# Kernel tuning notes

Hardware: AMD Instinct MI355X
Metric: run time of the kernel (lower is better)

Reference implementation:

```python
import jax, jax.numpy as jnp
import numpy as np

N_HEAD = 8


def setup_inputs() -> dict:
    key = jax.random.key(0)
    ks = jax.random.split(key, 8)
    v, b, c, h, w = 8, 4, 512, 16, 16
    s = 1.0 / np.sqrt(c).astype(np.float32)
    return {
        "q": jax.random.normal(ks[0], (v, b, c, h, w), jnp.float32),
        "kv": jax.random.normal(ks[1], (v, b, c, h, w), jnp.float32),
        "Wq": jax.random.normal(ks[2], (c, c), jnp.float32) * s,
        "bq": jnp.zeros((c,), jnp.float32),
        "Wkv": jax.random.normal(ks[3], (c, 2 * c), jnp.float32) * s,
        "bkv": jnp.zeros((2 * c,), jnp.float32),
        "Wp": jax.random.normal(ks[4], (c, c), jnp.float32) * s,
        "bp": jnp.zeros((c,), jnp.float32),
    }


def reference(q, kv, Wq, bq, Wkv, bkv, Wp, bp):
    vi, bi, ci, hi, wi = q.shape
    hw = hi * wi
    T = vi * hw
    hd = ci // N_HEAD

    # rearrange 'v b c h w -> b (v h w) c'
    xq = q.transpose(1, 0, 3, 4, 2).reshape(bi, T, ci)
    xkv = kv.transpose(1, 0, 3, 4, 2).reshape(bi, T, ci)

    qp = xq @ Wq + bq                      # [b, T, c]
    k, v_ = jnp.split(xkv @ Wkv + bkv, 2, axis=-1)

    def heads(x):
        return x.reshape(bi, T, N_HEAD, hd).transpose(0, 2, 1, 3)  # [b,h,T,d]

    qh, kh, vh = heads(qp), heads(k), heads(v_)

    att = jnp.einsum('bhqd,bhkd->bhqk', qh, kh) * (1.0 / np.sqrt(hd).astype(np.float32))

    # block-causal mask: query block (size h*w) may attend to key blocks <= its own
    blocks = jnp.arange(T) // hw
    mask = blocks[:, None] >= blocks[None, :]
    att = jnp.where(mask, att, -jnp.inf)
    att = jax.nn.softmax(att, axis=-1)

    y = jnp.einsum('bhqk,bhkd->bhqd', att, vh)
    y = y.transpose(0, 2, 1, 3).reshape(bi, T, ci)
    y = y @ Wp + bp

    # rearrange 'b (v h w) c -> v b c h w'
    return y.reshape(bi, vi, hi, wi, ci).transpose(1, 0, 4, 2, 3)
```

## Files before the change

kernel.cpp:

```cpp
#include <hip/hip_runtime.h>
#include <hip/hip_bf16.h>
#include <cmath>

typedef unsigned short u16;
typedef __attribute__((ext_vector_type(8))) short s8v;
typedef __attribute__((ext_vector_type(4))) float f4v;
typedef __attribute__((ext_vector_type(2))) float f2v;
typedef __attribute__((ext_vector_type(4))) unsigned int u32x4;
typedef __attribute__((ext_vector_type(4))) unsigned short u16x4;

#define MFMA(a,b,c) __builtin_amdgcn_mfma_f32_16x16x32_bf16((a),(b),(c),0,0,0)

__device__ __forceinline__ float bf2f(u16 u) {
    union { float f; unsigned i; } x; x.i = ((unsigned)u) << 16; return x.f;
}
__device__ __forceinline__ u16 f2bf(float f) {
    union { float f; unsigned i; } x; x.f = f;
    unsigned r = x.i + 0x7FFFu + ((x.i >> 16) & 1u);
    return (u16)(r >> 16);
}
__device__ __forceinline__ unsigned cvtpk(float lo, float hi) {
    unsigned r;
    asm("v_cvt_pk_bf16_f32 %0, %1, %2" : "=v"(r) : "v"(lo), "v"(hi));
    return r;
}
__device__ __forceinline__ void gload_lds16(const void* g, void* l) {
    __builtin_amdgcn_global_load_lds(
        (const __attribute__((address_space(1))) unsigned int*)g,
        (__attribute__((address_space(3))) unsigned int*)l, 16, 0, 0);
}
__device__ __forceinline__ int swb(int row, int colb) {
    return row * 128 + (colb ^ ((((row >> 4) ^ row) & 7) << 4));
}

__constant__ int CPER[8]  = {1,1,2,2,3,3,4,4};
__constant__ int POFF[17] = {0,1,2,3,4,6,8,10,12,15,18,21,24,28,32,36,40};

__global__ __launch_bounds__(256, 3)
void qkv_proj(const float* __restrict__ q, const float* __restrict__ kv,
              const float* __restrict__ Wq, const float* __restrict__ bq,
              const float* __restrict__ Wkv, const float* __restrict__ bkv,
              u16* __restrict__ QH, u16* __restrict__ KH, u16* __restrict__ VT)
{
    __shared__ __align__(16) u16 Tl[2][128 * 64];

    const int bid = blockIdx.x;
    const int x = bid & 7, i = bid >> 3;
    const int mt = x + 8 * (i / 12);
    const int nt = i % 12;
    const int m0 = mt << 7, n0 = nt << 7;

    const int tid  = threadIdx.x;
    const int lane = tid & 63;
    const int w    = tid >> 6;
    const int wr = (w >> 1) * 64, wc = (w & 1) * 64;
    const int cl = lane & 15, rl = lane >> 4;

    const int bb  = m0 >> 11;
    const int t0  = m0 & 2047;
    const int vv  = t0 >> 8;
    const int hw0 = t0 & 255;

    const float* Abase = ((nt < 4) ? q : kv) + (size_t)(vv * 4 + bb) * 131072 + hw0;

    const float* W; const float* bias; int NW, wn0, dn0; u16* dst;
    if (nt < 4)      { W = Wq;  bias = bq;  NW = 512;  wn0 = n0;       dn0 = n0;        dst = QH; }
    else if (nt < 8) { W = Wkv; bias = bkv; NW = 1024; wn0 = n0 - 512; dn0 = n0 - 512;  dst = KH; }
    else             { W = Wkv; bias = bkv; NW = 1024; wn0 = n0 - 512; dn0 = n0 - 1024; dst = VT; }

    const float oscale = (nt < 4) ? 0.18033688011f : 1.0f;

    f4v acc[4][4] = {};
    f2v la0[8], lb0[8], la1[8], lb1[8];

    const int mh = tid & 63;
    const int kb = tid >> 6;

#define QKV_LOAD(dA, dB, k0_) do {                                           \
        const float* gA = Abase + (size_t)((k0_) + kb * 8) * 256 + mh * 2;   \
        const float* gB = W + (size_t)((k0_) + kb * 8) * NW + wn0 + mh * 2;  \
        _Pragma("unroll")                                                    \
        for (int j = 0; j < 8; ++j) {                                        \
            dA[j] = *reinterpret_cast<const f2v*>(gA + j * 256);             \
            dB[j] = *reinterpret_cast<const f2v*>(gB + (size_t)j * NW);      \
        }                                                                    \
    } while (0)

#define QKV_WRITE(bufi, sA, sB) do {                                         \
        _Pragma("unroll")                                                    \
        for (int e = 0; e < 2; ++e) {                                        \
            u32x4 pa, pb;                                                    \
            _Pragma("unroll")                                                \
            for (int jj = 0; jj < 4; ++jj) {                                 \
                pa[jj] = cvtpk(sA[jj * 2][e], sA[jj * 2 + 1][e]);            \
                pb[jj] = cvtpk(sB[jj * 2][e], sB[jj * 2 + 1][e]);            \
            }                                                                \
            *(u32x4*)((char*)&Tl[bufi][0] + swb(mh * 2 + e, kb * 16)) = pa;  \
            *(u32x4*)((char*)&Tl[bufi][0] + swb(mh * 2 + e, 64 + kb * 16)) = pb; \
        }                                                                    \
    } while (0)

#define QKV_MFMA(bufi) do {                                                  \
        s8v af[4], bf[4];                                                    \
        _Pragma("unroll")                                                    \
        for (int mi = 0; mi < 4; ++mi)                                       \
            af[mi] = *(const s8v*)((const char*)&Tl[bufi][0]                 \
                                   + swb(wr + mi * 16 + cl, rl * 16));       \
        _Pragma("unroll")                                                    \
        for (int ni = 0; ni < 4; ++ni)                                       \
            bf[ni] = *(const s8v*)((const char*)&Tl[bufi][0]                 \
                                   + swb(wc + ni * 16 + cl, 64 + rl * 16));  \
        _Pragma("unroll")                                                    \
        for (int mi = 0; mi < 4; ++mi)                                       \
            _Pragma("unroll")                                                \
            for (int ni = 0; ni < 4; ++ni)                                   \
                acc[mi][ni] = MFMA(af[mi], bf[ni], acc[mi][ni]);             \
    } while (0)

    QKV_LOAD(la0, lb0, 0);
    QKV_WRITE(0, la0, lb0);
    QKV_LOAD(la1, lb1, 32);
    __syncthreads();

    #pragma unroll
    for (int it = 0; it < 8; ++it) {
        const int t = it * 2;
        QKV_WRITE(1, la1, lb1);
        if (t + 2 < 16) QKV_LOAD(la0, lb0, (t + 2) * 32);
        QKV_MFMA(0);
        __syncthreads();
        if (t + 2 < 16) QKV_WRITE(0, la0, lb0);
        if (t + 3 < 16) QKV_LOAD(la1, lb1, (t + 3) * 32);
        QKV_MFMA(1);
        __syncthreads();
    }
#undef QKV_LOAD
#undef QKV_WRITE
#undef QKV_MFMA

    if (nt < 8) {
        #pragma unroll
        for (int ni = 0; ni < 4; ++ni) {
            const int nl   = wc + ni * 16 + cl;
            const float bv = bias[wn0 + nl];
            const int cout = dn0 + nl;
            const int hh = cout >> 6, dd = cout & 63;
            const size_t obase = ((size_t)(bb * 8 + hh) * 2048) * 64 + dd;
            #pragma unroll
            for (int mi = 0; mi < 4; ++mi)
                #pragma unroll
                for (int r = 0; r < 4; ++r) {
                    const int m = m0 + wr + mi * 16 + rl * 4 + r;
                    const int t = m & 2047;
                    dst[obase + (size_t)t * 64] = f2bf((acc[mi][ni][r] + bv) * oscale);
                }
        }
    } else {
        #pragma unroll
        for (int ni = 0; ni < 4; ++ni) {
            const int nl   = wc + ni * 16 + cl;
            const float bv = bias[wn0 + nl];
            const int cout = dn0 + nl;
            const int hh = cout >> 6, dd = cout & 63;
            const size_t obase = ((size_t)(bb * 8 + hh) * 64 + dd) * 2048;
            #pragma unroll
            for (int mi = 0; mi < 4; ++mi) {
                const int m = m0 + wr + mi * 16 + rl * 4;
                const int t = m & 2047;
                u16x4 pk;
                #pragma unroll
                for (int r = 0; r < 4; ++r) pk[r] = f2bf(acc[mi][ni][r] + bv);
                *reinterpret_cast<u16x4*>(dst + obase + t) = pk;
            }
        }
    }
}

__global__ __launch_bounds__(256, 3)
void attn_part(const u16* __restrict__ QH, const u16* __restrict__ KH,
               const u16* __restrict__ VT,
               u16* __restrict__ Opart, float* __restrict__ ML)
{
    __shared__ __align__(16) u16 Kl[2][4096];
    __shared__ __align__(16) u16 Vl[2][4096];
    __shared__ u16 Pl[4][32][36];

    const int wg = blockIdx.x;
    const int bh = wg & 31;
    const int s  = 39 - (wg >> 5);
    int p = 0;
    #pragma unroll
    for (int i = 0; i < 15; ++i) p += (s >= POFF[i + 1]) ? 1 : 0;
    const int c  = s - POFF[p];
    const int qb = p >> 1;
    const int kstart = c * 512;
    const int nk = min(512, (qb + 1) * 256 - kstart);
    const int nt64 = nk >> 6;

    const int tid = threadIdx.x, lane = tid & 63, w = tid >> 6;
    const int cl = lane & 15, rl = lane >> 4;

    const u16* Qb = QH + (size_t)bh * 131072;
    const u16* Kb = KH + (size_t)bh * 131072;
    const u16* Vb = VT + (size_t)bh * 131072;

    const int qrow0 = p * 128 + w * 32;

    s8v qf[2][2];
    #pragma unroll
    for (int mi = 0; mi < 2; ++mi)
        #pragma unroll
        for (int kf = 0; kf < 2; ++kf)
            qf[mi][kf] = *reinterpret_cast<const s8v*>(
                Qb + (size_t)(qrow0 + mi * 16 + cl) * 64 + kf * 32 + rl * 8);

    unsigned kofs[2], vofs[2];
    #pragma unroll
    for (int i = 0; i < 2; ++i) {
        const int f = w * 128 + i * 64 + lane;
        const int row = f >> 3;
        kofs[i] = row * 128 + (((f & 7) * 16) ^ ((row & 7) << 4));
        vofs[i] = row * 4096 + (((f & 7) * 16) ^ ((row & 7) << 4));
    }

#define ISSUE(bufi, kb0_) do {                                               \
        const char* kG = (const char*)Kb + (size_t)(kb0_) * 128;             \
        const char* vG = (const char*)Vb + (size_t)(kb0_) * 2;               \
        char* kL = (char*)&Kl[bufi][0] + w * 2048;                           \
        char* vL = (char*)&Vl[bufi][0] + w * 2048;                           \
        _Pragma("unroll")                                                    \
        for (int i_ = 0; i_ < 2; ++i_) {                                     \
            gload_lds16(kG + kofs[i_], kL + i_ * 1024);                      \
            gload_lds16(vG + vofs[i_], vL + i_ * 1024);                      \
        }                                                                    \
    } while (0)

    f4v o[2][4] = {};
    float lp[8] = {0.f, 0.f, 0.f, 0.f, 0.f, 0.f, 0.f, 0.f};

    ISSUE(0, kstart);

    for (int kt = 0; kt < nt64; ++kt) {
        asm volatile("s_waitcnt vmcnt(0)" ::: "memory");
        __builtin_amdgcn_sched_barrier(0);
        __syncthreads();
        if (kt + 1 < nt64) ISSUE((kt + 1) & 1, kstart + (kt + 1) * 64);

        const char* Kbase = (const char*)&Kl[kt & 1][0];
        const char* Vbase = (const char*)&Vl[kt & 1][0];

        f4v sc[2][4] = {};
        #pragma unroll
        for (int ni = 0; ni < 4; ++ni)
            #pragma unroll
            for (int kf = 0; kf < 2; ++kf) {
                const int row = ni * 16 + cl;
                s8v kfr = *reinterpret_cast<const s8v*>(
                    Kbase + row * 128 + ((kf * 64 + rl * 16) ^ ((row & 7) << 4)));
                sc[0][ni] = MFMA(qf[0][kf], kfr, sc[0][ni]);
                sc[1][ni] = MFMA(qf[1][kf], kfr, sc[1][ni]);
            }

        #pragma unroll
        for (int mi = 0; mi < 2; ++mi)
            #pragma unroll
            for (int ni = 0; ni < 4; ++ni)
                #pragma unroll
                for (int r = 0; r < 4; ++r)
                    sc[mi][ni][r] = exp2f(sc[mi][ni][r]);
        #pragma unroll
        for (int mi = 0; mi < 2; ++mi)
            #pragma unroll
            for (int r = 0; r < 4; ++r)
                lp[mi * 4 + r] += sc[mi][0][r] + sc[mi][1][r]
                                + sc[mi][2][r] + sc[mi][3][r];

        #pragma unroll
        for (int kw = 0; kw < 2; ++kw) {
            #pragma unroll
            for (int mi = 0; mi < 2; ++mi)
                #pragma unroll
                for (int jj = 0; jj < 2; ++jj) {
                    const int ni = kw * 2 + jj;
                    const unsigned w0 = cvtpk(sc[mi][ni][0], sc[mi][ni][1]);
                    const unsigned w1 = cvtpk(sc[mi][ni][2], sc[mi][ni][3]);
                    const int col = jj * 16 + cl;
                    Pl[w][mi * 16 + rl * 4 + 0][col] = (u16)w0;
                    Pl[w][mi * 16 + rl * 4 + 1][col] = (u16)(w0 >> 16);
                    Pl[w][mi * 16 + rl * 4 + 2][col] = (u16)w1;
                    Pl[w][mi * 16 + rl * 4 + 3][col] = (u16)(w1 >> 16);
                }
            s8v pf0 = *reinterpret_cast<const s8v*>(&Pl[w][cl][rl * 8]);
            s8v pf1 = *reinterpret_cast<const s8v*>(&Pl[w][16 + cl][rl * 8]);
            #pragma unroll
            for (int di = 0; di < 4; ++di) {
                const int row = di * 16 + cl;
                s8v vf = *reinterpret_cast<const s8v*>(
                    Vbase + row * 128 + ((kw * 64 + rl * 16) ^ ((row & 7) << 4)));
                o[0][di] = MFMA(pf0, vf, o[0][di]);
                o[1][di] = MFMA(pf1, vf, o[1][di]);
            }
        }
    }
#undef ISSUE

    const int slot = bh * 40 + POFF[p] + c;
    #pragma unroll
    for (int mi = 0; mi < 2; ++mi)
        #pragma unroll
        for (int r = 0; r < 4; ++r) {
            const int idx = mi * 4 + r;
            float ls = lp[idx];
            ls += __shfl_xor(ls, 1);
            ls += __shfl_xor(ls, 2);
            ls += __shfl_xor(ls, 4);
            ls += __shfl_xor(ls, 8);
            const float inv = 1.f / ls;
            const int rloc = w * 32 + mi * 16 + rl * 4 + r;
            if (cl == 0) ML[(size_t)slot * 128 + rloc] = ls;
            #pragma unroll
            for (int di = 0; di < 4; ++di)
                Opart[(size_t)slot * 8192 + rloc * 64 + di * 16 + cl] =
                    f2bf(o[mi][di][r] * inv);
        }
}

__global__ __launch_bounds__(256)
void attn_combine(const u16* __restrict__ Opart, const float* __restrict__ ML,
                  u16* __restrict__ YH)
{
    const int wg = blockIdx.x;
    const int bh = wg & 31;
    const int p  = wg >> 5;
    const int b = bh >> 3, h = bh & 7;
    const int nc = CPER[p >> 1];
    const int sb = bh * 40 + POFF[p];

    const int t = threadIdx.x;
    const int rloc = t >> 1;
    const int dh = (t & 1) * 32;

    float lc[4], L = 0.f;
    for (int c = 0; c < nc; ++c) {
        lc[c] = ML[(size_t)(sb + c) * 128 + rloc];
        L += lc[c];
    }
    const float invL = 1.f / L;
    float wgt[4];
    for (int c = 0; c < nc; ++c) wgt[c] = lc[c] * invL;

    f4v a[8] = {};
    for (int c = 0; c < nc; ++c) {
        const float wv = wgt[c];
        #pragma unroll
        for (int u = 0; u < 4; ++u) {
            s8v vv = *reinterpret_cast<const s8v*>(
                &Opart[(size_t)(sb + c) * 8192 + rloc * 64 + dh + u * 8]);
            #pragma unroll
            for (int e = 0; e < 4; ++e) a[u * 2][e]     += wv * bf2f((u16)vv[e]);
            #pragma unroll
            for (int e = 0; e < 4; ++e) a[u * 2 + 1][e] += wv * bf2f((u16)vv[e + 4]);
        }
    }

    const size_t ybase = ((size_t)b * 2048 + p * 128 + rloc) * 512 + h * 64 + dh;
    #pragma unroll
    for (int u = 0; u < 4; ++u) {
        s8v ov;
        #pragma unroll
        for (int e = 0; e < 4; ++e) ov[e]     = (short)f2bf(a[u * 2][e]);
        #pragma unroll
        for (int e = 0; e < 4; ++e) ov[e + 4] = (short)f2bf(a[u * 2 + 1][e]);
        *reinterpret_cast<s8v*>(YH + ybase + u * 8) = ov;
    }
}

__global__ __launch_bounds__(256)
void out_proj(const u16* __restrict__ YH, const float* __restrict__ Wp,
              const float* __restrict__ bp, float* __restrict__ out)
{
    __shared__ __align__(16) u16 Al[2][128 * 64];
    __shared__ u16 Bl[2][128][40];

    const int bid = blockIdx.x;
    const int x = bid & 7, i = bid >> 3;
    const int mt = x + 8 * (i >> 2);
    const int ct = i & 3;
    const int c0 = ct << 7, m0 = mt << 7;

    const int tid = threadIdx.x, lane = tid & 63, w = tid >> 6;
    const int wr = (w >> 1) * 64, wc = (w & 1) * 64;
    const int cl = lane & 15, rl = lane >> 4;

    f4v acc[4][4] = {};
    f2v wa0[8], wa1[8];
    s8v sy0[2], sy1[2];

    const int mh = tid & 63;
    const int kb = tid >> 6;
    const int br = tid >> 2;
    const int bq4 = (tid & 3) * 8;

#define OP_LOAD(dA, dY, k0_) do {                                            \
        const float* gA = Wp + (size_t)((k0_) + kb * 8) * 512 + c0 + mh * 2; \
        _Pragma("unroll")                                                    \
        for (int j = 0; j < 8; ++j)                                          \
            dA[j] = *reinterpret_cast<const f2v*>(gA + j * 512);             \
        _Pragma("unroll")                                                    \
        for (int it = 0; it < 2; ++it)                                       \
            dY[it] = *reinterpret_cast<const s8v*>(                          \
                YH + (size_t)(m0 + br + it * 64) * 512 + (k0_) + bq4);       \
    } while (0)

#define OP_WRITE(bufi, sA, sY) do {                                          \
        _Pragma("unroll")                                                    \
        for (int e = 0; e < 2; ++e) {                                        \
            u32x4 pa;                                                        \
            _Pragma("unroll")                                                \
            for (int jj = 0; jj < 4; ++jj)                                   \
                pa[jj] = cvtpk(sA[jj * 2][e], sA[jj * 2 + 1][e]);            \
            *(u32x4*)((char*)&Al[bufi][0] + swb(mh * 2 + e, kb * 16)) = pa;  \
        }                                                                    \
        _Pragma("unroll")                                                    \
        for (int it = 0; it < 2; ++it)                                       \
            *reinterpret_cast<s8v*>(&Bl[bufi][br + it * 64][bq4]) = sY[it];  \
    } while (0)

#define OP_MFMA(bufi) do {                                                   \
        s8v af[4], bfr[4];                                                   \
        _Pragma("unroll")                                                    \
        for (int mi = 0; mi < 4; ++mi)                                       \
            af[mi] = *(const s8v*)((const char*)&Al[bufi][0]                 \
                                   + swb(wr + mi * 16 + cl, rl * 16));       \
        _Pragma("unroll")                                                    \
        for (int ni = 0; ni < 4; ++ni)                                       \
            bfr[ni] = *reinterpret_cast<const s8v*>(                         \
                &Bl[bufi][wc + ni * 16 + cl][rl * 8]);                       \
        _Pragma("unroll")                                                    \
        for (int mi = 0; mi < 4; ++mi)                                       \
            _Pragma("unroll")                                                \
            for (int ni = 0; ni < 4; ++ni)                                   \
                acc[mi][ni] = MFMA(af[mi], bfr[ni], acc[mi][ni]);            \
    } while (0)

    OP_LOAD(wa0, sy0, 0);
    OP_WRITE(0, wa0, sy0);
    OP_LOAD(wa1, sy1, 32);
    __syncthreads();

    #pragma unroll
    for (int it = 0; it < 8; ++it) {
        const int t = it * 2;
        OP_WRITE(1, wa1, sy1);
        if (t + 2 < 16) OP_LOAD(wa0, sy0, (t + 2) * 32);
        OP_MFMA(0);
        __syncthreads();
        if (t + 2 < 16) OP_WRITE(0, wa0, sy0);
        if (t + 3 < 16) OP_LOAD(wa1, sy1, (t + 3) * 32);
        OP_MFMA(1);
        __syncthreads();
    }
#undef OP_LOAD
#undef OP_WRITE
#undef OP_MFMA

    #pragma unroll
    for (int mi = 0; mi < 4; ++mi)
        #pragma unroll
        for (int r = 0; r < 4; ++r) {
            const int c = c0 + wr + mi * 16 + rl * 4 + r;
            const float bv = bp[c];
            #pragma unroll
            for (int ni = 0; ni < 4; ++ni) {
                const int tok = m0 + wc + ni * 16 + cl;
                const int bb = tok >> 11, t = tok & 2047;
                const int vv = t >> 8, hw = t & 255;
                out[(size_t)(vv * 4 + bb) * 131072 + (size_t)c * 256 + hw] =
                    acc[mi][ni][r] + bv;
            }
        }
}

extern "C" void kernel_launch(void* const* d_in, const int* in_sizes, int n_in,
                              void* d_out, int out_size, void* d_ws, size_t ws_size,
                              hipStream_t stream)
{
    const float* q   = (const float*)d_in[0];
    const float* kv  = (const float*)d_in[1];
    const float* Wq  = (const float*)d_in[2];
    const float* bq  = (const float*)d_in[3];
    const float* Wkv = (const float*)d_in[4];
    const float* bkv = (const float*)d_in[5];
    const float* Wp  = (const float*)d_in[6];
    const float* bp  = (const float*)d_in[7];
    float* out = (float*)d_out;

    u16* ws = (u16*)d_ws;
    u16* QH = ws;
    u16* KH = QH + 4194304;
    u16* VT = KH + 4194304;
    u16* YH = VT + 4194304;
    u16* Opart = YH + 4194304;
    float* ML  = (float*)(Opart + 10485760);

    hipLaunchKernelGGL(qkv_proj, dim3(768), dim3(256), 0, stream,
                       q, kv, Wq, bq, Wkv, bkv, QH, KH, VT);
    hipLaunchKernelGGL(attn_part, dim3(1280), dim3(256), 0, stream,
                       QH, KH, VT, Opart, ML);
    hipLaunchKernelGGL(attn_combine, dim3(512), dim3(256), 0, stream,
                       Opart, ML, YH);
    hipLaunchKernelGGL(out_proj, dim3(256), dim3(256), 0, stream, YH, Wp, bp, out);
}
```

Measured before the change: 103.8 us.

## Enlarge attention query tile to one full view block with 512-thread workgroups

The attention partial kernel now handles 256 query rows (a whole view block) per workgroup using 8 waves instead of 128 rows with 4 waves. This halves the number of workgroups and the K/V tile loads per query row, since each staged 64-key tile is shared by twice as many queries. Each thread now issues one async LDS load per tensor per tile. The partition tables and the combine kernel's indexing are updated to match. In exchange there are fewer workgroups (640) and larger per-block LDS use, which may reduce occupancy and load balance across the causal partitions.

```diff
diff --git a/kernel.cpp b/kernel.cpp
--- a/kernel.cpp
+++ b/kernel.cpp
@@ -33,8 +33,8 @@
     return row * 128 + (colb ^ ((((row >> 4) ^ row) & 7) << 4));
 }
 
-__constant__ int CPER[8]  = {1,1,2,2,3,3,4,4};
-__constant__ int POFF[17] = {0,1,2,3,4,6,8,10,12,15,18,21,24,28,32,36,40};
+__constant__ int CPER2[8]  = {1,1,2,2,3,3,4,4};
+__constant__ int POFF2[9]  = {0,1,2,4,6,9,12,16,20};
 
 __global__ __launch_bounds__(256, 3)
 void qkv_proj(const float* __restrict__ q, const float* __restrict__ kv,
@@ -176,25 +176,24 @@
     }
 }
 
-__global__ __launch_bounds__(256, 3)
+__global__ __launch_bounds__(512, 6)
 void attn_part(const u16* __restrict__ QH, const u16* __restrict__ KH,
                const u16* __restrict__ VT,
                u16* __restrict__ Opart, float* __restrict__ ML)
 {
     __shared__ __align__(16) u16 Kl[2][4096];
     __shared__ __align__(16) u16 Vl[2][4096];
-    __shared__ u16 Pl[4][32][36];
+    __shared__ u16 Pl[8][32][36];
 
     const int wg = blockIdx.x;
     const int bh = wg & 31;
-    const int s  = 39 - (wg >> 5);
+    const int s  = 19 - (wg >> 5);
     int p = 0;
     #pragma unroll
-    for (int i = 0; i < 15; ++i) p += (s >= POFF[i + 1]) ? 1 : 0;
-    const int c  = s - POFF[p];
-    const int qb = p >> 1;
+    for (int i = 0; i < 7; ++i) p += (s >= POFF2[i + 1]) ? 1 : 0;
+    const int c  = s - POFF2[p];
     const int kstart = c * 512;
-    const int nk = min(512, (qb + 1) * 256 - kstart);
+    const int nk = min(512, (p + 1) * 256 - kstart);
     const int nt64 = nk >> 6;
 
     const int tid = threadIdx.x, lane = tid & 63, w = tid >> 6;
@@ -204,7 +203,7 @@
     const u16* Kb = KH + (size_t)bh * 131072;
     const u16* Vb = VT + (size_t)bh * 131072;
 
-    const int qrow0 = p * 128 + w * 32;
+    const int qrow0 = p * 256 + w * 32;
 
     s8v qf[2][2];
     #pragma unroll
@@ -214,25 +213,15 @@
             qf[mi][kf] = *reinterpret_cast<const s8v*>(
                 Qb + (size_t)(qrow0 + mi * 16 + cl) * 64 + kf * 32 + rl * 8);
 
-    unsigned kofs[2], vofs[2];
-    #pragma unroll
-    for (int i = 0; i < 2; ++i) {
-        const int f = w * 128 + i * 64 + lane;
-        const int row = f >> 3;
-        kofs[i] = row * 128 + (((f & 7) * 16) ^ ((row & 7) << 4));
-        vofs[i] = row * 4096 + (((f & 7) * 16) ^ ((row & 7) << 4));
-    }
+    const int fr = tid >> 3, fc = (tid & 7) * 16;
+    const unsigned kofs = fr * 128 + (fc ^ ((fr & 7) << 4));
+    const unsigned vofs = fr * 4096 + (fc ^ ((fr & 7) << 4));
 
 #define ISSUE(bufi, kb0_) do {                                               \
-        const char* kG = (const char*)Kb + (size_t)(kb0_) * 128;             \
-        const char* vG = (const char*)Vb + (size_t)(kb0_) * 2;               \
-        char* kL = (char*)&Kl[bufi][0] + w * 2048;                           \
-        char* vL = (char*)&Vl[bufi][0] + w * 2048;                           \
-        _Pragma("unroll")                                                    \
-        for (int i_ = 0; i_ < 2; ++i_) {                                     \
-            gload_lds16(kG + kofs[i_], kL + i_ * 1024);                      \
-            gload_lds16(vG + vofs[i_], vL + i_ * 1024);                      \
-        }                                                                    \
+        gload_lds16((const char*)Kb + (size_t)(kb0_) * 128 + kofs,           \
+                    (char*)&Kl[bufi][0] + w * 1024);                         \
+        gload_lds16((const char*)Vb + (size_t)(kb0_) * 2 + vofs,             \
+                    (char*)&Vl[bufi][0] + w * 1024);                         \
     } while (0)
 
     f4v o[2][4] = {};
@@ -304,7 +293,7 @@
     }
 #undef ISSUE
 
-    const int slot = bh * 40 + POFF[p] + c;
+    const int slot = bh * 20 + POFF2[p] + c;
     #pragma unroll
     for (int mi = 0; mi < 2; ++mi)
         #pragma unroll
@@ -317,10 +306,10 @@
             ls += __shfl_xor(ls, 8);
             const float inv = 1.f / ls;
             const int rloc = w * 32 + mi * 16 + rl * 4 + r;
-            if (cl == 0) ML[(size_t)slot * 128 + rloc] = ls;
+            if (cl == 0) ML[(size_t)slot * 256 + rloc] = ls;
             #pragma unroll
             for (int di = 0; di < 4; ++di)
-                Opart[(size_t)slot * 8192 + rloc * 64 + di * 16 + cl] =
+                Opart[(size_t)slot * 16384 + rloc * 64 + di * 16 + cl] =
                     f2bf(o[mi][di][r] * inv);
         }
 }
@@ -331,18 +320,19 @@
 {
     const int wg = blockIdx.x;
     const int bh = wg & 31;
-    const int p  = wg >> 5;
+    const int p  = (wg >> 5) & 7;
+    const int half = wg >> 8;
     const int b = bh >> 3, h = bh & 7;
-    const int nc = CPER[p >> 1];
-    const int sb = bh * 40 + POFF[p];
+    const int nc = CPER2[p];
+    const int sb = bh * 20 + POFF2[p];
 
     const int t = threadIdx.x;
-    const int rloc = t >> 1;
+    const int rloc = (t >> 1) + half * 128;
     const int dh = (t & 1) * 32;
 
     float lc[4], L = 0.f;
     for (int c = 0; c < nc; ++c) {
-        lc[c] = ML[(size_t)(sb + c) * 128 + rloc];
+        lc[c] = ML[(size_t)(sb + c) * 256 + rloc];
         L += lc[c];
     }
     const float invL = 1.f / L;
@@ -355,7 +345,7 @@
         #pragma unroll
         for (int u = 0; u < 4; ++u) {
             s8v vv = *reinterpret_cast<const s8v*>(
-                &Opart[(size_t)(sb + c) * 8192 + rloc * 64 + dh + u * 8]);
+                &Opart[(size_t)(sb + c) * 16384 + rloc * 64 + dh + u * 8]);
             #pragma unroll
             for (int e = 0; e < 4; ++e) a[u * 2][e]     += wv * bf2f((u16)vv[e]);
             #pragma unroll
@@ -363,7 +353,7 @@
         }
     }
 
-    const size_t ybase = ((size_t)b * 2048 + p * 128 + rloc) * 512 + h * 64 + dh;
+    const size_t ybase = ((size_t)b * 2048 + p * 256 + rloc) * 512 + h * 64 + dh;
     #pragma unroll
     for (int u = 0; u < 4; ++u) {
         s8v ov;
@@ -505,7 +495,7 @@
 
     hipLaunchKernelGGL(qkv_proj, dim3(768), dim3(256), 0, stream,
                        q, kv, Wq, bq, Wkv, bkv, QH, KH, VT);
-    hipLaunchKernelGGL(attn_part, dim3(1280), dim3(256), 0, stream,
+    hipLaunchKernelGGL(attn_part, dim3(640), dim3(512), 0, stream,
                        QH, KH, VT, Opart, ML);
     hipLaunchKernelGGL(attn_combine, dim3(512), dim3(256), 0, stream,
                        Opart, ML, YH);
```

After: 167.5 us. 1.61x slower.
